# Kernel optimization log

Measured on AMD Instinct MI355X. Metric: run time of the kernel, lower is better.

Reference implementation:

```python
import jax, jax.numpy as jnp
import numpy as np

V = 100000   # vocab_size
E = 300      # embedding_dim
H = 512      # hidden_dim
HH = H // 2  # per-direction hidden
T = 24       # tagset size (incl START/STOP)
START, STOP = 22, 23
S = 4096     # sentence length
NEG = -10000.0


def setup_inputs() -> dict:
    key = jax.random.key(0)
    ks = jax.random.split(key, 12)
    sc = 0.05
    trans = jax.random.normal(ks[10], (T, T), jnp.float32) * 0.01
    # no transition INTO START, none OUT OF STOP (tutorial convention: trans[to, from])
    trans = trans.at[START, :].set(NEG).at[:, STOP].set(NEG)
    return {
        "sentence": jax.random.randint(ks[0], (S,), 0, V),
        "emb_table": jax.random.normal(ks[1], (V, E), jnp.float32) * sc,
        "w_ih_f": jax.random.normal(ks[2], (4 * HH, E), jnp.float32) * sc,
        "w_hh_f": jax.random.normal(ks[3], (4 * HH, HH), jnp.float32) * sc,
        "b_f": jnp.zeros((4 * HH,), jnp.float32),
        "w_ih_b": jax.random.normal(ks[4], (4 * HH, E), jnp.float32) * sc,
        "w_hh_b": jax.random.normal(ks[5], (4 * HH, HH), jnp.float32) * sc,
        "b_b": jnp.zeros((4 * HH,), jnp.float32),
        "w_tag": jax.random.normal(ks[6], (T, H), jnp.float32) * sc,
        "b_tag": jnp.zeros((T,), jnp.float32),
        "transitions": trans,
    }


def _lstm(x, w_ih, w_hh, b, reverse):
    # PyTorch LSTM gate order: i, f, g, o
    def step(carry, xt):
        h, c = carry
        g = xt @ w_ih.T + h @ w_hh.T + b
        i, f, gg, o = jnp.split(g, 4)
        c = jax.nn.sigmoid(f) * c + jax.nn.sigmoid(i) * jnp.tanh(gg)
        h = jax.nn.sigmoid(o) * jnp.tanh(c)
        return (h, c), h
    init = (jnp.zeros((HH,), x.dtype), jnp.zeros((HH,), x.dtype))
    _, hs = jax.lax.scan(step, init, x, reverse=reverse)
    return hs  # [S, HH], in original time order for both directions


def reference(sentence, emb_table, w_ih_f, w_hh_f, b_f, w_ih_b, w_hh_b, b_b,
              w_tag, b_tag, transitions):
    x = emb_table[sentence]                                   # [S, E]
    h = jnp.concatenate([_lstm(x, w_ih_f, w_hh_f, b_f, False),
                         _lstm(x, w_ih_b, w_hh_b, b_b, True)], axis=-1)  # [S, H]
    feats = h @ w_tag.T + b_tag                               # [S, T] emissions

    # Viterbi decode (tutorial _viterbi_decode)
    vinit = jnp.full((T,), NEG, feats.dtype).at[START].set(0.0)

    def vstep(v, feat):
        scores = v[None, :] + transitions                     # [to, from]
        return jnp.max(scores, axis=1) + feat, jnp.argmax(scores, axis=1)

    v, bptrs = jax.lax.scan(vstep, vinit, feats)              # bptrs: [S, T]
    term = v + transitions[STOP]
    best = jnp.argmax(term)
    score = term[best]

    def back(tag, bp):
        return bp[tag], tag

    _, path = jax.lax.scan(back, best, bptrs, reverse=True)   # [S] best tag seq
    return score, path
```

## Files before the change

kernel.cpp:

```cpp
#include <hip/hip_runtime.h>
#include <hip/hip_bf16.h>

#define S_LEN 4096
#define NTAG 24
#define START_TAG 22
#define STOP_TAG 23
#define SENT 0x7F800001u

static const size_t OFF_WT    = 0;
static const size_t OFF_XG    = OFF_WT + (size_t)300*2048*4;
static const size_t OFF_HS    = OFF_XG + (size_t)2*4096*1024*4;
static const size_t OFF_FEATS = OFF_HS + (size_t)2*4096*256*4;
static const size_t OFF_BP    = OFF_FEATS + (size_t)4096*24*4;
static const size_t OFF_WALK  = OFF_XG;

__device__ __forceinline__ float sigf(float x) {
    return __fdividef(1.f, 1.f + __expf(-x));
}
__device__ __forceinline__ float tanhfast(float x) {
    return 1.f - __fdividef(2.f, 1.f + __expf(2.f * x));
}

__device__ __forceinline__ float atomic_poll_word(const float* p) {
    float v;
    do {
        v = __hip_atomic_load(p, __ATOMIC_RELAXED, __HIP_MEMORY_SCOPE_AGENT);
    } while (__float_as_uint(v) == SENT);
    return v;
}

__global__ void prep_kernel(const float* __restrict__ w_ih_f, const float* __restrict__ w_ih_b,
                            float* __restrict__ WT, unsigned int* __restrict__ HSu) {
    int tid = blockIdx.x * blockDim.x + threadIdx.x;
    int nth = gridDim.x * blockDim.x;
    for (int idx = tid; idx < 300 * 2048; idx += nth) {
        int k = idx / 2048, col = idx % 2048;
        WT[idx] = (col < 1024) ? w_ih_f[col * 300 + k] : w_ih_b[(col - 1024) * 300 + k];
    }
    for (int idx = tid; idx < 2 * S_LEN * 256; idx += nth)
        HSu[idx] = SENT;
}

__global__ __launch_bounds__(256) void embed_xg_kernel(const int* __restrict__ sentence,
                                                       const float* __restrict__ emb,
                                                       const float* __restrict__ WT,
                                                       const float* __restrict__ b_f,
                                                       const float* __restrict__ b_b,
                                                       float* __restrict__ xg) {
    __shared__ float xs[16][300];
    int s0 = blockIdx.x * 16;
    for (int idx = threadIdx.x; idx < 16 * 300; idx += 256) {
        int si = idx / 300, k = idx - si * 300;
        int wrow = sentence[s0 + si];
        xs[si][k] = emb[(size_t)wrow * 300 + k];
    }
    __syncthreads();
    for (int chunk = 0; chunk < 8; ++chunk) {
        int col = chunk * 256 + threadIdx.x;
        float acc[16];
#pragma unroll
        for (int s = 0; s < 16; ++s) acc[s] = 0.f;
        for (int k = 0; k < 300; k += 4) {
            float w0 = WT[(k + 0) * 2048 + col];
            float w1 = WT[(k + 1) * 2048 + col];
            float w2 = WT[(k + 2) * 2048 + col];
            float w3 = WT[(k + 3) * 2048 + col];
#pragma unroll
            for (int s = 0; s < 16; ++s) {
                float4 x4 = *reinterpret_cast<const float4*>(&xs[s][k]);
                acc[s] += w0 * x4.x + w1 * x4.y + w2 * x4.z + w3 * x4.w;
            }
        }
        int dir = col >> 10;
        int row = col & 1023;
        float bias = dir ? b_b[row] : b_f[row];
#pragma unroll
        for (int s = 0; s < 16; ++s)
            xg[((size_t)dir * S_LEN + (s0 + s)) * 1024 + row] = acc[s] + bias;
    }
}

__global__ __launch_bounds__(1024) void lstm_kernel(const float* __restrict__ xg,
                                                    const float* __restrict__ w_hh_f,
                                                    const float* __restrict__ w_hh_b,
                                                    float* __restrict__ hs) {
    const int xslot = blockIdx.x & 7;
    if (xslot > 1) return;
    const int dir = xslot;
    const int blk = blockIdx.x >> 3;
    const int tid = threadIdx.x;
    const int r4 = tid >> 5;
    const int kc = tid & 31;

    __shared__ float hsk[32 * 10];
    __shared__ float part[128][33];
    __shared__ float gl[128];

    const float* whh = dir ? w_hh_b : w_hh_f;
    float w[4][8];
#pragma unroll
    for (int q = 0; q < 4; ++q) {
        int R = r4 * 4 + q;
        int grow = ((R >> 5) << 8) + blk * 32 + (R & 31);
#pragma unroll
        for (int j = 0; j < 8; ++j)
            w[q][j] = whh[(size_t)grow * 256 + kc * 8 + j];
    }

    for (int i = tid; i < 320; i += 1024) hsk[i] = 0.f;

    const float* xgd = xg + (size_t)dir * S_LEN * 1024;
    float* hsd = hs + (size_t)dir * S_LEN * 256;
    float c = 0.f;

    int growR = 0;
    float xg_cur = 0.f;
    const bool is_red = (tid >= 512 && tid < 640);
    if (is_red) {
        const int l = tid - 512;
        growR = ((l >> 5) << 8) + blk * 32 + (l & 31);
        xg_cur = xgd[(size_t)(dir ? (S_LEN - 1) : 0) * 1024 + growR];
    }
    const bool is_pol = (tid >= 256 && tid < 512) && (((tid - 256) >> 5) != blk);
    const int pol_w = ((tid - 256) >> 5) * 32 + (tid & 31);
    __syncthreads();

    for (int step = 0; step < S_LEN; ++step) {
        const int st = dir ? (S_LEN - 1 - step) : step;

        float hv[8];
        const int hb = kc * 10;
#pragma unroll
        for (int j = 0; j < 8; ++j) hv[j] = hsk[hb + j];
        float p0 = 0.f, p1 = 0.f, p2 = 0.f, p3 = 0.f;
#pragma unroll
        for (int j = 0; j < 8; ++j) {
            p0 += w[0][j] * hv[j];
            p1 += w[1][j] * hv[j];
            p2 += w[2][j] * hv[j];
            p3 += w[3][j] * hv[j];
        }
        part[r4 * 4 + 0][kc] = p0;
        part[r4 * 4 + 1][kc] = p1;
        part[r4 * 4 + 2][kc] = p2;
        part[r4 * 4 + 3][kc] = p3;
        __syncthreads();

        float xg_nxt = 0.f;
        if (is_red) {
            const int l = tid - 512;
            if (step + 1 < S_LEN) {
                const int stn = dir ? (st - 1) : (st + 1);
                xg_nxt = xgd[(size_t)stn * 1024 + growR];
            }
            float a0 = 0.f, a1 = 0.f, a2 = 0.f, a3 = 0.f;
#pragma unroll
            for (int k2 = 0; k2 < 32; k2 += 4) {
                a0 += part[l][k2 + 0];
                a1 += part[l][k2 + 1];
                a2 += part[l][k2 + 2];
                a3 += part[l][k2 + 3];
            }
            gl[l] = xg_cur + ((a0 + a1) + (a2 + a3));
        }
        __syncthreads();

        if (tid < 32) {
            float gi = gl[tid], gf = gl[32 + tid], gg = gl[64 + tid], go = gl[96 + tid];
            float si = sigf(gi), sf = sigf(gf), so = sigf(go);
            c = sf * c + si * tanhfast(gg);
            float h = so * tanhfast(c);
            __hip_atomic_store(&hsd[(size_t)st * 256 + blk * 32 + tid], h,
                               __ATOMIC_RELAXED, __HIP_MEMORY_SCOPE_AGENT);
            int w0 = blk * 32 + tid;
            hsk[(w0 >> 3) * 10 + (w0 & 7)] = h;
        }
        else if (is_pol && step + 1 < S_LEN) {
            float v = atomic_poll_word(&hsd[(size_t)st * 256 + pol_w]);
            hsk[(pol_w >> 3) * 10 + (pol_w & 7)] = v;
        }
        xg_cur = xg_nxt;
        __syncthreads();
    }
}

__global__ __launch_bounds__(384) void feats_kernel(const float* __restrict__ hs,
                                                    const float* __restrict__ w_tag,
                                                    const float* __restrict__ b_tag,
                                                    float* __restrict__ feats) {
    __shared__ float ht[16][512];
    int s0 = blockIdx.x * 16;
    for (int idx = threadIdx.x; idx < 16 * 512; idx += 384) {
        int si = idx >> 9, k = idx & 511;
        float v = (k < 256) ? hs[(size_t)(s0 + si) * 256 + k]
                            : hs[(size_t)S_LEN * 256 + (size_t)(s0 + si) * 256 + (k - 256)];
        ht[si][k] = v;
    }
    __syncthreads();
    int si = threadIdx.x / NTAG;
    int t = threadIdx.x - si * NTAG;
    float acc = b_tag[t];
    const float* wr = w_tag + t * 512;
    for (int k = 0; k < 512; k += 4) {
        float4 w4 = *reinterpret_cast<const float4*>(&wr[k]);
        float4 h4 = *reinterpret_cast<const float4*>(&ht[si][k]);
        acc += w4.x * h4.x + w4.y * h4.y + w4.z * h4.z + w4.w * h4.w;
    }
    feats[(size_t)(s0 + si) * NTAG + t] = acc;
}

__global__ __launch_bounds__(1024) void viterbi_kernel(const float* __restrict__ feats,
                                                       const float* __restrict__ trans,
                                                       unsigned char* __restrict__ bp_g,
                                                       unsigned char* __restrict__ walk_g,
                                                       float* __restrict__ out) {
    const int tid = threadIdx.x;
    __shared__ float s_bv;
    __shared__ int s_bti;
    __shared__ unsigned char maps[32][24];
    __shared__ int Bc[32];

    if (tid < 64) {
        const int lane = tid;
        const bool lo = lane < NTAG;
        const bool hi = (lane >= 32) && (lane < 32 + NTAG);
        const bool act = lo || hi;
        const int to = lo ? lane : lane - 32;
        const int fbase = lo ? 0 : 12;
        float wt[12];
#pragma unroll
        for (int j = 0; j < 12; ++j)
            wt[j] = act ? trans[to * NTAG + fbase + j] : -3.0e38f;
        float v = act ? ((to == START_TAG) ? 0.f : -10000.f) : -3.0e38f;
        float feat = act ? feats[to] : 0.f;

        for (int s = 0; s < S_LEN; ++s) {
            float featn = (act && s + 1 < S_LEN) ? feats[(s + 1) * NTAG + to] : 0.f;
            float m1 = -3.0e38f;
            int b1 = fbase;
#pragma unroll
            for (int j = 0; j < 12; ++j) {
                float cand = __shfl(v, fbase + j) + wt[j];
                if (cand > m1) { m1 = cand; b1 = fbase + j; }
            }
            float m2 = __shfl_xor(m1, 32);
            int b2 = __shfl_xor(b1, 32);
            float mlo = lo ? m1 : m2; int blo = lo ? b1 : b2;
            float mhi = lo ? m2 : m1; int bhi = lo ? b2 : b1;
            float m = fmaxf(mlo, mhi);
            int bi = (mhi > mlo) ? bhi : blo;
            v = m + feat;
            if (lo) bp_g[s * NTAG + lane] = (unsigned char)bi;
            feat = featn;
        }
        float wstop = act ? trans[STOP_TAG * NTAG + to] : 0.f;
        float bv = lo ? (v + wstop) : -3.0e38f;
        int bti = lo ? lane : 64;
#pragma unroll
        for (int d = 1; d < 64; d <<= 1) {
            float ov = __shfl_xor(bv, d);
            int oi = __shfl_xor(bti, d);
            if (ov > bv || (ov == bv && oi < bti)) { bv = ov; bti = oi; }
        }
        if (lane == 0) { s_bv = bv; s_bti = bti; }
    }
    __syncthreads();

    if (tid < 32 * NTAG) {
        const int c = tid / NTAG, E = tid - c * NTAG;
        const unsigned char* bpc = bp_g + (size_t)c * 128 * NTAG;
        unsigned char* wk = walk_g + (size_t)(c * NTAG + E) * 128;
        int m = E;
        wk[127] = (unsigned char)m;
        for (int j = 126; j >= 0; --j) {
            m = bpc[(j + 1) * NTAG + m];
            wk[j] = (unsigned char)m;
        }
        maps[c][E] = bpc[m];
    }
    __syncthreads();

    if (tid == 0) {
        int t = s_bti;
        for (int c = 31; c >= 0; --c) {
            Bc[c] = t;
            if (c) t = maps[c][t];
        }
        out[0] = s_bv;
    }
    __syncthreads();

    for (int i = tid; i < S_LEN; i += 1024) {
        int c = i >> 7, j = i & 127;
        out[1 + i] = (float)walk_g[(size_t)(c * NTAG + Bc[c]) * 128 + j];
    }
}

extern "C" void kernel_launch(void* const* d_in, const int* in_sizes, int n_in,
                              void* d_out, int out_size, void* d_ws, size_t ws_size,
                              hipStream_t stream) {
    const int*   sentence = (const int*)d_in[0];
    const float* emb      = (const float*)d_in[1];
    const float* w_ih_f   = (const float*)d_in[2];
    const float* w_hh_f   = (const float*)d_in[3];
    const float* b_f      = (const float*)d_in[4];
    const float* w_ih_b   = (const float*)d_in[5];
    const float* w_hh_b   = (const float*)d_in[6];
    const float* b_b      = (const float*)d_in[7];
    const float* w_tag    = (const float*)d_in[8];
    const float* b_tag    = (const float*)d_in[9];
    const float* trans    = (const float*)d_in[10];

    char* ws = (char*)d_ws;
    float*         WT    = (float*)(ws + OFF_WT);
    float*         XG    = (float*)(ws + OFF_XG);
    float*         HS    = (float*)(ws + OFF_HS);
    float*         FEATS = (float*)(ws + OFF_FEATS);
    unsigned char* BP    = (unsigned char*)(ws + OFF_BP);
    unsigned char* WALK  = (unsigned char*)(ws + OFF_WALK);

    float* out = (float*)d_out;

    prep_kernel<<<512, 256, 0, stream>>>(w_ih_f, w_ih_b, WT, (unsigned int*)HS);
    embed_xg_kernel<<<S_LEN / 16, 256, 0, stream>>>(sentence, emb, WT, b_f, b_b, XG);
    lstm_kernel<<<64, 1024, 0, stream>>>(XG, w_hh_f, w_hh_b, HS);
    feats_kernel<<<S_LEN / 16, 384, 0, stream>>>(HS, w_tag, b_tag, FEATS);
    viterbi_kernel<<<1, 1024, 0, stream>>>(FEATS, trans, BP, WALK, out);
}
```

Before: 8.770 ms.

## Replace LDS partial-sum reduction with warp shuffles and fuse gate math per row

The recurrent LSTM step now reduces the 32 per-lane dot-product partials with butterfly xor shuffles inside each 32-lane group, so the lane with kc==31 holds full gate sums and computes the cell update directly. This removes the part[] and gl[] shared buffers and one of the three block barriers per time step, shortening the serial per-step critical path. The x-gate prefetch moves to a double-buffered LDS slot filled by the last 128 threads. Polling of other blocks' h values is redistributed across threads so that lanes with kc==31, which now do gate work, are not also pollers.

Result: slower. 12.45 ms (+42.0%).

```diff
diff --git a/kernel.cpp b/kernel.cpp
--- a/kernel.cpp
+++ b/kernel.cpp
@@ -89,19 +89,17 @@
     const int dir = xslot;
     const int blk = blockIdx.x >> 3;
     const int tid = threadIdx.x;
-    const int r4 = tid >> 5;
+    const int rq = tid >> 5;
     const int kc = tid & 31;
 
-    __shared__ float hsk[32 * 10];
-    __shared__ float part[128][33];
-    __shared__ float gl[128];
+    __shared__ float hsk[320];
+    __shared__ float xgl[2][128];
 
     const float* whh = dir ? w_hh_b : w_hh_f;
     float w[4][8];
 #pragma unroll
     for (int q = 0; q < 4; ++q) {
-        int R = r4 * 4 + q;
-        int grow = ((R >> 5) << 8) + blk * 32 + (R & 31);
+        int grow = q * 256 + blk * 32 + rq;
 #pragma unroll
         for (int j = 0; j < 8; ++j)
             w[q][j] = whh[(size_t)grow * 256 + kc * 8 + j];
@@ -111,27 +109,39 @@
 
     const float* xgd = xg + (size_t)dir * S_LEN * 1024;
     float* hsd = hs + (size_t)dir * S_LEN * 256;
+
+    int widx = -1;
+    if (tid < 256) {
+        int g = tid >> 5;
+        if (g != blk && kc != 31) widx = g * 32 + kc;
+    } else if (tid < 264) {
+        int g = tid - 256;
+        if (g != blk) widx = g * 32 + 31;
+    }
+    const bool is_stage = (tid >= 896);
+    const int sl = tid - 896;
+    int growS = 0;
+    if (is_stage) growS = ((sl >> 5) << 8) + blk * 32 + (sl & 31);
+    const bool is_gate = (kc == 31);
     float c = 0.f;
 
-    int growR = 0;
-    float xg_cur = 0.f;
-    const bool is_red = (tid >= 512 && tid < 640);
-    if (is_red) {
-        const int l = tid - 512;
-        growR = ((l >> 5) << 8) + blk * 32 + (l & 31);
-        xg_cur = xgd[(size_t)(dir ? (S_LEN - 1) : 0) * 1024 + growR];
-    }
-    const bool is_pol = (tid >= 256 && tid < 512) && (((tid - 256) >> 5) != blk);
-    const int pol_w = ((tid - 256) >> 5) * 32 + (tid & 31);
+    if (is_stage)
+        xgl[0][sl] = xgd[(size_t)(dir ? (S_LEN - 1) : 0) * 1024 + growS];
     __syncthreads();
 
     for (int step = 0; step < S_LEN; ++step) {
         const int st = dir ? (S_LEN - 1 - step) : step;
+        const int par = step & 1;
+
+        float xg_pre = 0.f;
+        if (is_stage && step + 1 < S_LEN) {
+            const int stn = dir ? (st - 1) : (st + 1);
+            xg_pre = xgd[(size_t)stn * 1024 + growS];
+        }
 
         float hv[8];
-        const int hb = kc * 10;
-#pragma unroll
-        for (int j = 0; j < 8; ++j) hv[j] = hsk[hb + j];
+#pragma unroll
+        for (int j = 0; j < 8; ++j) hv[j] = hsk[kc * 10 + j];
         float p0 = 0.f, p1 = 0.f, p2 = 0.f, p3 = 0.f;
 #pragma unroll
         for (int j = 0; j < 8; ++j) {
@@ -140,46 +150,37 @@
             p2 += w[2][j] * hv[j];
             p3 += w[3][j] * hv[j];
         }
-        part[r4 * 4 + 0][kc] = p0;
-        part[r4 * 4 + 1][kc] = p1;
-        part[r4 * 4 + 2][kc] = p2;
-        part[r4 * 4 + 3][kc] = p3;
+#pragma unroll
+        for (int d = 1; d < 32; d <<= 1) {
+            p0 += __shfl_xor(p0, d);
+            p1 += __shfl_xor(p1, d);
+            p2 += __shfl_xor(p2, d);
+            p3 += __shfl_xor(p3, d);
+        }
+
+        float h = 0.f;
+        if (is_gate) {
+            float gi = p0 + xgl[par][rq];
+            float gf = p1 + xgl[par][32 + rq];
+            float gg = p2 + xgl[par][64 + rq];
+            float go = p3 + xgl[par][96 + rq];
+            c = sigf(gf) * c + sigf(gi) * tanhfast(gg);
+            h = sigf(go) * tanhfast(c);
+            __hip_atomic_store(&hsd[(size_t)st * 256 + blk * 32 + rq], h,
+                               __ATOMIC_RELAXED, __HIP_MEMORY_SCOPE_AGENT);
+        }
         __syncthreads();
 
-        float xg_nxt = 0.f;
-        if (is_red) {
-            const int l = tid - 512;
-            if (step + 1 < S_LEN) {
-                const int stn = dir ? (st - 1) : (st + 1);
-                xg_nxt = xgd[(size_t)stn * 1024 + growR];
-            }
-            float a0 = 0.f, a1 = 0.f, a2 = 0.f, a3 = 0.f;
-#pragma unroll
-            for (int k2 = 0; k2 < 32; k2 += 4) {
-                a0 += part[l][k2 + 0];
-                a1 += part[l][k2 + 1];
-                a2 += part[l][k2 + 2];
-                a3 += part[l][k2 + 3];
-            }
-            gl[l] = xg_cur + ((a0 + a1) + (a2 + a3));
-        }
-        __syncthreads();
-
-        if (tid < 32) {
-            float gi = gl[tid], gf = gl[32 + tid], gg = gl[64 + tid], go = gl[96 + tid];
-            float si = sigf(gi), sf = sigf(gf), so = sigf(go);
-            c = sf * c + si * tanhfast(gg);
-            float h = so * tanhfast(c);
-            __hip_atomic_store(&hsd[(size_t)st * 256 + blk * 32 + tid], h,
-                               __ATOMIC_RELAXED, __HIP_MEMORY_SCOPE_AGENT);
-            int w0 = blk * 32 + tid;
+        if (is_gate) {
+            int w0 = blk * 32 + rq;
             hsk[(w0 >> 3) * 10 + (w0 & 7)] = h;
         }
-        else if (is_pol && step + 1 < S_LEN) {
-            float v = atomic_poll_word(&hsd[(size_t)st * 256 + pol_w]);
-            hsk[(pol_w >> 3) * 10 + (pol_w & 7)] = v;
-        }
-        xg_cur = xg_nxt;
+        if (widx >= 0 && step + 1 < S_LEN) {
+            float v = atomic_poll_word(&hsd[(size_t)st * 256 + widx]);
+            hsk[(widx >> 3) * 10 + (widx & 7)] = v;
+        }
+        if (is_stage && step + 1 < S_LEN)
+            xgl[par ^ 1][sl] = xg_pre;
         __syncthreads();
     }
 }
```

## Restructure LSTM recurrence to drop one barrier per step and shorten the reduction

Applied to the files above, without the earlier changes.

Each of the 16 waves now holds 32 recurrent weights for one row and one 32-wide k-slice, giving 8 partial sums per gate row instead of 32. The gate threads sum these partials directly, which removes the separate reduction stage and one __syncthreads per time step. The next step's input-gate loads move into the gate threads, and pollers are remapped to a contiguous range of threads. More registers per thread and a longer dot product per thread are traded for fewer barriers on the serial critical path.

Result: no change. 8.890 ms (+1.4%).

```diff
diff --git a/kernel.cpp b/kernel.cpp
--- a/kernel.cpp
+++ b/kernel.cpp
@@ -89,97 +89,91 @@
     const int dir = xslot;
     const int blk = blockIdx.x >> 3;
     const int tid = threadIdx.x;
-    const int r4 = tid >> 5;
-    const int kc = tid & 31;
-
-    __shared__ float hsk[32 * 10];
-    __shared__ float part[128][33];
-    __shared__ float gl[128];
+    const int wv = tid >> 6;
+    const int l  = tid & 63;
+    const int s  = wv >> 1;
+    const int hi = wv & 1;
+    const int r  = hi * 64 + l;
+
+    __shared__ float hvec[256];
+    __shared__ float part[128][9];
 
     const float* whh = dir ? w_hh_b : w_hh_f;
-    float w[4][8];
-#pragma unroll
-    for (int q = 0; q < 4; ++q) {
-        int R = r4 * 4 + q;
-        int grow = ((R >> 5) << 8) + blk * 32 + (R & 31);
-#pragma unroll
-        for (int j = 0; j < 8; ++j)
-            w[q][j] = whh[(size_t)grow * 256 + kc * 8 + j];
-    }
-
-    for (int i = tid; i < 320; i += 1024) hsk[i] = 0.f;
+    const int g = r >> 5, j = r & 31;
+    const int grow = g * 256 + blk * 32 + j;
+    float w[32];
+#pragma unroll
+    for (int i = 0; i < 32; ++i)
+        w[i] = whh[(size_t)grow * 256 + s * 32 + i];
+
+    for (int i = tid; i < 256; i += 1024) hvec[i] = 0.f;
 
     const float* xgd = xg + (size_t)dir * S_LEN * 1024;
     float* hsd = hs + (size_t)dir * S_LEN * 256;
     float c = 0.f;
 
-    int growR = 0;
-    float xg_cur = 0.f;
-    const bool is_red = (tid >= 512 && tid < 640);
-    if (is_red) {
-        const int l = tid - 512;
-        growR = ((l >> 5) << 8) + blk * 32 + (l & 31);
-        xg_cur = xgd[(size_t)(dir ? (S_LEN - 1) : 0) * 1024 + growR];
-    }
-    const bool is_pol = (tid >= 256 && tid < 512) && (((tid - 256) >> 5) != blk);
-    const int pol_w = ((tid - 256) >> 5) * 32 + (tid & 31);
+    const bool is_gate = (tid < 32);
+    float xc0 = 0.f, xc1 = 0.f, xc2 = 0.f, xc3 = 0.f;
+    if (is_gate) {
+        const size_t b0 = (size_t)(dir ? (S_LEN - 1) : 0) * 1024 + blk * 32 + tid;
+        xc0 = xgd[b0];
+        xc1 = xgd[b0 + 256];
+        xc2 = xgd[b0 + 512];
+        xc3 = xgd[b0 + 768];
+    }
+    const bool is_pol = (tid >= 64 && tid < 288);
+    int pol_w = 0;
+    if (is_pol) {
+        int idx = tid - 64;
+        pol_w = idx + ((idx >= blk * 32) ? 32 : 0);
+    }
     __syncthreads();
 
     for (int step = 0; step < S_LEN; ++step) {
         const int st = dir ? (S_LEN - 1 - step) : step;
 
-        float hv[8];
-        const int hb = kc * 10;
-#pragma unroll
-        for (int j = 0; j < 8; ++j) hv[j] = hsk[hb + j];
-        float p0 = 0.f, p1 = 0.f, p2 = 0.f, p3 = 0.f;
-#pragma unroll
-        for (int j = 0; j < 8; ++j) {
-            p0 += w[0][j] * hv[j];
-            p1 += w[1][j] * hv[j];
-            p2 += w[2][j] * hv[j];
-            p3 += w[3][j] * hv[j];
-        }
-        part[r4 * 4 + 0][kc] = p0;
-        part[r4 * 4 + 1][kc] = p1;
-        part[r4 * 4 + 2][kc] = p2;
-        part[r4 * 4 + 3][kc] = p3;
+        float xn0 = 0.f, xn1 = 0.f, xn2 = 0.f, xn3 = 0.f;
+        if (is_gate && step + 1 < S_LEN) {
+            const int stn = dir ? (st - 1) : (st + 1);
+            const size_t bn = (size_t)stn * 1024 + blk * 32 + tid;
+            xn0 = xgd[bn];
+            xn1 = xgd[bn + 256];
+            xn2 = xgd[bn + 512];
+            xn3 = xgd[bn + 768];
+        }
+
+        float a0 = 0.f, a1 = 0.f, a2 = 0.f, a3 = 0.f;
+#pragma unroll
+        for (int i4 = 0; i4 < 8; ++i4) {
+            float4 h4 = *reinterpret_cast<const float4*>(&hvec[s * 32 + i4 * 4]);
+            a0 += w[i4 * 4 + 0] * h4.x;
+            a1 += w[i4 * 4 + 1] * h4.y;
+            a2 += w[i4 * 4 + 2] * h4.z;
+            a3 += w[i4 * 4 + 3] * h4.w;
+        }
+        part[r][s] = (a0 + a1) + (a2 + a3);
         __syncthreads();
 
-        float xg_nxt = 0.f;
-        if (is_red) {
-            const int l = tid - 512;
-            if (step + 1 < S_LEN) {
-                const int stn = dir ? (st - 1) : (st + 1);
-                xg_nxt = xgd[(size_t)stn * 1024 + growR];
+        if (is_gate) {
+            float g0 = xc0, g1 = xc1, g2 = xc2, g3 = xc3;
+#pragma unroll
+            for (int ss = 0; ss < 8; ++ss) {
+                g0 += part[tid][ss];
+                g1 += part[32 + tid][ss];
+                g2 += part[64 + tid][ss];
+                g3 += part[96 + tid][ss];
             }
-            float a0 = 0.f, a1 = 0.f, a2 = 0.f, a3 = 0.f;
-#pragma unroll
-            for (int k2 = 0; k2 < 32; k2 += 4) {
-                a0 += part[l][k2 + 0];
-                a1 += part[l][k2 + 1];
-                a2 += part[l][k2 + 2];
-                a3 += part[l][k2 + 3];
-            }
-            gl[l] = xg_cur + ((a0 + a1) + (a2 + a3));
-        }
-        __syncthreads();
-
-        if (tid < 32) {
-            float gi = gl[tid], gf = gl[32 + tid], gg = gl[64 + tid], go = gl[96 + tid];
-            float si = sigf(gi), sf = sigf(gf), so = sigf(go);
-            c = sf * c + si * tanhfast(gg);
-            float h = so * tanhfast(c);
+            c = sigf(g1) * c + sigf(g0) * tanhfast(g2);
+            float h = sigf(g3) * tanhfast(c);
             __hip_atomic_store(&hsd[(size_t)st * 256 + blk * 32 + tid], h,
                                __ATOMIC_RELAXED, __HIP_MEMORY_SCOPE_AGENT);
-            int w0 = blk * 32 + tid;
-            hsk[(w0 >> 3) * 10 + (w0 & 7)] = h;
+            hvec[blk * 32 + tid] = h;
         }
         else if (is_pol && step + 1 < S_LEN) {
             float v = atomic_poll_word(&hsd[(size_t)st * 256 + pol_w]);
-            hsk[(pol_w >> 3) * 10 + (pol_w & 7)] = v;
-        }
-        xg_cur = xg_nxt;
+            hvec[pol_w] = v;
+        }
+        xc0 = xn0; xc1 = xn1; xc2 = xn2; xc3 = xn3;
         __syncthreads();
     }
 }
```
